# Kernel tuning notes

Hardware: AMD Instinct MI355X
Metric: run time of the kernel (lower is better)

## Reference

```python
import jax, jax.numpy as jnp
import numpy as np

N = 262144   # nodes
E = 1048576  # edges (avg degree 4)
DIN = 64     # input node features
H = 128      # hidden channels
DE = 32      # edge feature dim
EPS = 1e-5


def setup_inputs() -> dict:
    key = jax.random.key(0)
    ks = jax.random.split(key, 12)
    s = 0.05
    return {
        "x": jax.random.normal(ks[0], (N, DIN), jnp.float32),
        "edge_attr": jax.random.normal(ks[1], (E, DE), jnp.float32),
        "W_enter": jax.random.normal(ks[2], (H, DIN), jnp.float32) * s,
        "b_enter": jnp.zeros((H,), jnp.float32),
        "W1": jax.random.normal(ks[3], (H, H + DE), jnp.float32) * s,
        "att_l": jax.random.normal(ks[4], (H,), jnp.float32) * s,
        "att_r": jax.random.normal(ks[5], (H,), jnp.float32) * s,
        "W2": jax.random.normal(ks[6], (H, H), jnp.float32) * s,
        "b_conv": jnp.zeros((H,), jnp.float32),
        "W_ih": jax.random.normal(ks[7], (3 * H, H), jnp.float32) * s,
        "W_hh": jax.random.normal(ks[8], (3 * H, H), jnp.float32) * s,
        "b_ih": jnp.zeros((3 * H,), jnp.float32),
        "b_hh": jnp.zeros((3 * H,), jnp.float32),
        "edge_index": jax.random.randint(ks[9], (2, E), 0, N, jnp.int32),
    }


def _segment_softmax(logits, seg, num_segments):
    m = jax.ops.segment_max(logits, seg, num_segments=num_segments)
    e = jnp.exp(logits - m[seg])
    d = jax.ops.segment_sum(e, seg, num_segments=num_segments)
    return e / d[seg]


def reference(x, edge_attr, W_enter, b_enter, W1, att_l, att_r, W2, b_conv,
              W_ih, W_hh, b_ih, b_hh, edge_index):
    n = x.shape[0]
    src, dst = edge_index[0], edge_index[1]  # x_j = x[src], aggregate to dst

    # lin_enter + leaky_relu
    x = jax.nn.leaky_relu(x @ W_enter.T + b_enter)

    # Edge2dConv message: leaky_relu(lin1([x_j, edge_attr]))
    m = jax.nn.leaky_relu(jnp.concatenate([x[src], edge_attr], axis=-1) @ W1.T)  # [E,H]
    alpha = jax.nn.leaky_relu(m @ att_l + x[dst] @ att_r)  # [E]
    alpha = _segment_softmax(alpha, dst, n)
    msg = (m @ W2.T) * alpha[:, None]
    out = jax.ops.segment_sum(msg, dst, num_segments=n) + b_conv

    # elu, then GRUCell(h_in=out_elu, hidden=x)
    h = jax.nn.elu(out)
    gi = h @ W_ih.T + b_ih
    gh = x @ W_hh.T + b_hh
    ir, iz, inn = jnp.split(gi, 3, axis=-1)
    hr, hz, hn = jnp.split(gh, 3, axis=-1)
    r = jax.nn.sigmoid(ir + hr)
    z = jax.nn.sigmoid(iz + hz)
    ncand = jnp.tanh(inn + r * hn)
    x = jax.nn.relu((1.0 - z) * ncand + z * x)

    # layer_norm (no affine)
    mu = jnp.mean(x, axis=-1, keepdims=True)
    var = jnp.mean(jnp.square(x - mu), axis=-1, keepdims=True)
    return (x - mu) / jnp.sqrt(var + EPS)
```

## Files before the change

### kernel.cpp

```cpp
#include <hip/hip_runtime.h>
#include <stdint.h>

#define HD  128
#define DIN 64
#define DE  32

typedef unsigned int u32; typedef unsigned short u16; typedef unsigned char u8;
typedef long i64_;
typedef short s16x8 __attribute__((ext_vector_type(8)));
typedef float f32x4 __attribute__((ext_vector_type(4)));
typedef float f32x2 __attribute__((ext_vector_type(2)));

#define MFMA16(a,b,c)  __builtin_amdgcn_mfma_f32_16x16x32_bf16((a),(b),(c),0,0,0)
#define MFMAF8(a,b,c)  __builtin_amdgcn_mfma_f32_16x16x32_fp8_fp8((a),(b),(c),0,0,0)

__device__ __forceinline__ float lrelu(float x){ return x > 0.f ? x : 0.01f*x; }
__device__ __forceinline__ float sigmoidf_(float x){ return 1.f/(1.f + __expf(-x)); }
__device__ __forceinline__ float tanhf_(float x){
    float t = fminf(fmaxf(x, -15.f), 15.f);
    float e = __expf(2.f*t);
    return (e - 1.f)/(e + 1.f);
}
__device__ __forceinline__ float eluf_(float x){ return x > 0.f ? x : expm1f(x); }

__device__ __forceinline__ u16 f32_to_bf16(float x){
    u32 u = __float_as_uint(x);
    u += 0x7FFFu + ((u >> 16) & 1u);
    return (u16)(u >> 16);
}
__device__ __forceinline__ float bf16lo(u32 u){ return __uint_as_float((u & 0xFFFFu) << 16); }
__device__ __forceinline__ float bf16hi(u32 u){ return __uint_as_float(u & 0xFFFF0000u); }
__device__ __forceinline__ float bf16f(u16 h){ return __uint_as_float(((u32)h) << 16); }
__device__ __forceinline__ u32 pk2(float a, float b){
    return (u32)f32_to_bf16(a) | ((u32)f32_to_bf16(b) << 16);
}
__device__ __forceinline__ u8 hw_f8(float v){
    return (u8)__builtin_amdgcn_cvt_pk_fp8_f32(v, v, 0, false);
}
__device__ __forceinline__ u32 hw_f8x4(float a, float b, float c, float d){
    u32 r = (u32)__builtin_amdgcn_cvt_pk_fp8_f32(a, b, 0, false);
    r = (u32)__builtin_amdgcn_cvt_pk_fp8_f32(c, d, (int)r, true);
    return r;
}
__device__ __forceinline__ f32x2 hw_f8_dec2(u32 u){
    return __builtin_amdgcn_cvt_pk_f32_fp8((int)u, false);
}
__device__ __forceinline__ f32x2 hw_f8_dec2_hi(u32 u){
    return __builtin_amdgcn_cvt_pk_f32_fp8((int)u, true);
}

__device__ __forceinline__ float wave_max(float v){
    #pragma unroll
    for (int o = 32; o > 0; o >>= 1) v = fmaxf(v, __shfl_xor(v, o, 64));
    return v;
}
__device__ __forceinline__ float wave_sum(float v){
    #pragma unroll
    for (int o = 32; o > 0; o >>= 1) v += __shfl_xor(v, o, 64);
    return v;
}
__device__ __forceinline__ float dot8_bf16(uint4 v, const float* __restrict__ al){
    float d = 0.f;
    d = fmaf(bf16lo(v.x), al[0], d); d = fmaf(bf16hi(v.x), al[1], d);
    d = fmaf(bf16lo(v.y), al[2], d); d = fmaf(bf16hi(v.y), al[3], d);
    d = fmaf(bf16lo(v.z), al[4], d); d = fmaf(bf16hi(v.z), al[5], d);
    d = fmaf(bf16lo(v.w), al[6], d); d = fmaf(bf16hi(v.w), al[7], d);
    return d;
}

__global__ void k_prep(const float* __restrict__ W1, const float* __restrict__ W2,
                       const float* __restrict__ Went,
                       const float* __restrict__ Wih, const float* __restrict__ Whh,
                       u16* __restrict__ W1b, u16* __restrict__ W2b,
                       u16* __restrict__ Wentb, u8* __restrict__ Bgf8)
{
    int i = blockIdx.x*256 + threadIdx.x;
    if (i < 20480){ W1b[i] = f32_to_bf16(W1[i]); return; }
    i -= 20480;
    if (i < 16384){ W2b[i] = f32_to_bf16(W2[i]); return; }
    i -= 16384;
    if (i < 8192){ Wentb[i] = f32_to_bf16(Went[i]); return; }
    i -= 8192;
    if (i < 131072){
        int col = i >> 8, k = i & 255;
        int g = col >> 7, j = col & 127;
        float v;
        if      (g == 0) v = (k < 128) ? Wih[j*128 + k]        : Whh[j*128 + k - 128];
        else if (g == 1) v = (k < 128) ? Wih[(128+j)*128 + k]  : Whh[(128+j)*128 + k - 128];
        else if (g == 2) v = (k < 128) ? Wih[(256+j)*128 + k]  : 0.f;
        else             v = (k < 128) ? 0.f                   : Whh[(256+j)*128 + k - 128];
        Bgf8[i] = hw_f8(v);
    }
}

__global__ __launch_bounds__(256, 2) void k_enter_mfma(
    const float* __restrict__ x, const u16* __restrict__ Wb, const float* __restrict__ be,
    const float* __restrict__ att_r, u16* __restrict__ xeb, u8* __restrict__ Agru,
    float* __restrict__ r_out, int N)
{
    __shared__ __align__(16) u8 sA[64*144];
    __shared__ __align__(16) u8 sO[64*272];
    int t = threadIdx.x, w = t >> 6, lane = t & 63, l15 = lane & 15, l4 = lane >> 4;
    int tile = blockIdx.x;

    s16x8 bfr[2][2];
    #pragma unroll
    for (int kf = 0; kf < 2; ++kf)
        #pragma unroll
        for (int cf = 0; cf < 2; ++cf)
            bfr[kf][cf] = *(const s16x8*)(Wb + (size_t)(w*32 + cf*16 + l15)*64 + kf*32 + l4*8);

    int el = t >> 2, q = t & 3;
    size_t n = (size_t)tile*64 + el;
    {
        const float4* xs = (const float4*)(x + n*64 + q*16);
        float4 f0 = xs[0], f1 = xs[1], f2 = xs[2], f3 = xs[3];
        uint4 o0, o1;
        o0.x = pk2(f0.x,f0.y); o0.y = pk2(f0.z,f0.w); o0.z = pk2(f1.x,f1.y); o0.w = pk2(f1.z,f1.w);
        o1.x = pk2(f2.x,f2.y); o1.y = pk2(f2.z,f2.w); o1.z = pk2(f3.x,f3.y); o1.w = pk2(f3.z,f3.w);
        *(uint4*)(sA + el*144 + q*32)      = o0;
        *(uint4*)(sA + el*144 + q*32 + 16) = o1;
    }
    __syncthreads();

    f32x4 acc[4][2];
    #pragma unroll
    for (int rf = 0; rf < 4; ++rf){ acc[rf][0] = (f32x4)0.f; acc[rf][1] = (f32x4)0.f; }
    #pragma unroll
    for (int kf = 0; kf < 2; ++kf){
        s16x8 a[4];
        #pragma unroll
        for (int rf = 0; rf < 4; ++rf)
            a[rf] = *(const s16x8*)(sA + (rf*16 + l15)*144 + kf*64 + l4*16);
        #pragma unroll
        for (int rf = 0; rf < 4; ++rf){
            acc[rf][0] = MFMA16(a[rf], bfr[kf][0], acc[rf][0]);
            acc[rf][1] = MFMA16(a[rf], bfr[kf][1], acc[rf][1]);
        }
    }
    float b0 = be[w*32 + l15], b1 = be[w*32 + 16 + l15];
    #pragma unroll
    for (int rf = 0; rf < 4; ++rf)
        #pragma unroll
        for (int r = 0; r < 4; ++r){
            int row = rf*16 + l4*4 + r;
            *(u16*)(sO + row*272 + (w*32 + l15)*2)      = f32_to_bf16(lrelu(acc[rf][0][r] + b0));
            *(u16*)(sO + row*272 + (w*32 + 16 + l15)*2) = f32_to_bf16(lrelu(acc[rf][1][r] + b1));
        }
    __syncthreads();

    float dot = 0.f;
    #pragma unroll
    for (int i = 0; i < 4; ++i){
        uint4 v = *(const uint4*)(sO + el*272 + q*64 + 16*i);
        ((uint4*)xeb)[n*16 + q*4 + i] = v;
        float f0 = bf16lo(v.x), f1 = bf16hi(v.x), f2 = bf16lo(v.y), f3 = bf16hi(v.y);
        float f4 = bf16lo(v.z), f5 = bf16hi(v.z), f6 = bf16lo(v.w), f7 = bf16hi(v.w);
        const float* al = att_r + q*32 + 8*i;
        dot = fmaf(f0, al[0], dot); dot = fmaf(f1, al[1], dot);
        dot = fmaf(f2, al[2], dot); dot = fmaf(f3, al[3], dot);
        dot = fmaf(f4, al[4], dot); dot = fmaf(f5, al[5], dot);
        dot = fmaf(f6, al[6], dot); dot = fmaf(f7, al[7], dot);
        uint2 p; p.x = hw_f8x4(f0, f1, f2, f3); p.y = hw_f8x4(f4, f5, f6, f7);
        *(uint2*)(Agru + n*256 + 128 + q*32 + i*8) = p;
    }
    dot += __shfl_xor(dot, 1); dot += __shfl_xor(dot, 2);
    if (q == 0) r_out[n] = dot;
}

__global__ void k_hist(const int* __restrict__ dst, int* __restrict__ deg, int E){
    int e = blockIdx.x*256 + threadIdx.x;
    if (e < E) atomicAdd(&deg[dst[e]], 1);
}
__global__ __launch_bounds__(256) void k_scan_a(
    const int* __restrict__ deg, int* __restrict__ rs, int* __restrict__ btot, int N)
{
    __shared__ int sd[256];
    int b = blockIdx.x, t = threadIdx.x;
    int base = b*1024 + t*4;
    int d0 = deg[base], d1 = deg[base+1], d2 = deg[base+2], d3 = deg[base+3];
    int s = d0 + d1 + d2 + d3;
    sd[t] = s; __syncthreads();
    for (int o = 1; o < 256; o <<= 1){
        int v = (t >= o) ? sd[t-o] : 0;
        __syncthreads();
        sd[t] += v;
        __syncthreads();
    }
    int ex = sd[t] - s;
    rs[base]   = ex;
    rs[base+1] = ex + d0;
    rs[base+2] = ex + d0 + d1;
    rs[base+3] = ex + d0 + d1 + d2;
    if (t == 0) btot[b] = sd[255];
}
__global__ __launch_bounds__(256) void k_scan_b(const int* __restrict__ btot, int* __restrict__ bbase){
    __shared__ int sd[256];
    int t = threadIdx.x;
    int s = btot[t];
    sd[t] = s; __syncthreads();
    for (int o = 1; o < 256; o <<= 1){
        int v = (t >= o) ? sd[t-o] : 0;
        __syncthreads();
        sd[t] += v;
        __syncthreads();
    }
    bbase[t] = sd[t] - s;
}
__global__ void k_scan_c(int* __restrict__ rs, const int* __restrict__ bbase, int N, int E){
    int i = blockIdx.x*256 + threadIdx.x;
    if (i < N) rs[i] += bbase[i >> 10];
    if (i == 0) rs[N] = E;
}
__global__ void k_scatter(const int* __restrict__ dst, const int* __restrict__ rs,
                          int* __restrict__ cnt, int* __restrict__ epos, int E){
    int e = blockIdx.x*256 + threadIdx.x;
    if (e >= E) return;
    int d = dst[e];
    int pos = rs[d] + atomicAdd(&cnt[d], 1);
    epos[e] = pos;
}

__global__ __launch_bounds__(512, 4) void k_edge_mfma(
    const u16* __restrict__ xeb, const float* __restrict__ ea,
    const u16* __restrict__ W1b, const float* __restrict__ att_l,
    const float* __restrict__ r_dst, const int* __restrict__ src, const int* __restrict__ dst,
    const int* __restrict__ epos,
    u8* __restrict__ m, float* __restrict__ alpha, int ntiles, int E)
{
    __shared__ __align__(16) u8 sA[64*336];
    __shared__ __align__(16) u8 sM[64*144];
    int t = threadIdx.x, w = t >> 6, lane = t & 63, l15 = lane & 15, l4 = lane >> 4;

    s16x8 bfr[5];
    #pragma unroll
    for (int kf = 0; kf < 5; ++kf)
        bfr[kf] = *(const s16x8*)(W1b + (size_t)(w*16 + l15)*160 + kf*32 + l4*8);

    int el = t >> 3, q = t & 7;
    int stride = gridDim.x;
    int tile = blockIdx.x;

    uint4 cx0, cx1;
    u32 ce0, ce1;
    int   pe = 0;
    float rdv = 0.f;
    {
        int e = tile*64 + el;
        if (tile < ntiles && e < E){
            int sn = src[e];
            const uint4* xs = (const uint4*)xeb + (size_t)sn*16 + q*2;
            cx0 = xs[0]; cx1 = xs[1];
            float4 f = *(const float4*)(ea + (size_t)e*32 + q*4);
            ce0 = pk2(f.x, f.y); ce1 = pk2(f.z, f.w);
            pe  = epos[e];
            rdv = r_dst[dst[e]];
        }
    }

    int   ptile = -1;
    int   pe_prev = 0;
    float rdv_prev = 0.f;

    for (; tile < ntiles; tile += stride){
        int e = tile*64 + el;
        if (e < E){
            uint4* d = (uint4*)(sA + el*336 + q*32);
            d[0] = cx0; d[1] = cx1;
            *(u32*)(sA + el*336 + 256 + q*8)     = ce0;
            *(u32*)(sA + el*336 + 256 + q*8 + 4) = ce1;
        }
        int pe_cur = pe; float rdv_cur = rdv;

        int nt = tile + stride;
        if (nt < ntiles){
            int e2 = nt*64 + el;
            if (e2 < E){
                int sn = src[e2];
                const uint4* xs = (const uint4*)xeb + (size_t)sn*16 + q*2;
                cx0 = xs[0]; cx1 = xs[1];
                float4 f = *(const float4*)(ea + (size_t)e2*32 + q*4);
                ce0 = pk2(f.x, f.y); ce1 = pk2(f.z, f.w);
                pe  = epos[e2];
                rdv = r_dst[dst[e2]];
            }
        }

        if (ptile >= 0){
            int ep = ptile*64 + el;
            if (ep < E){
                uint4 v = *(const uint4*)(sM + el*144 + q*16);
                ((uint4*)m)[(size_t)pe_prev*8 + q] = v;
                u32 ws[4] = {v.x, v.y, v.z, v.w};
                float dotv = 0.f;
                #pragma unroll
                for (int i = 0; i < 4; ++i){
                    f32x2 fa = hw_f8_dec2(ws[i]);
                    f32x2 fb = hw_f8_dec2_hi(ws[i]);
                    const float* al = att_l + q*16 + i*4;
                    dotv = fmaf(fa.x, al[0], dotv); dotv = fmaf(fa.y, al[1], dotv);
                    dotv = fmaf(fb.x, al[2], dotv); dotv = fmaf(fb.y, al[3], dotv);
                }
                dotv += __shfl_xor(dotv, 1); dotv += __shfl_xor(dotv, 2); dotv += __shfl_xor(dotv, 4);
                if (q == 0) alpha[pe_prev] = lrelu(dotv + rdv_prev);
            }
        }
        __syncthreads();

        f32x4 acc[4];
        #pragma unroll
        for (int rf = 0; rf < 4; ++rf) acc[rf] = (f32x4)0.f;
        #pragma unroll
        for (int kf = 0; kf < 5; ++kf){
            s16x8 a[4];
            #pragma unroll
            for (int rf = 0; rf < 4; ++rf)
                a[rf] = *(const s16x8*)(sA + (rf*16 + l15)*336 + kf*64 + l4*16);
            #pragma unroll
            for (int rf = 0; rf < 4; ++rf)
                acc[rf] = MFMA16(a[rf], bfr[kf], acc[rf]);
        }

        int col = w*16 + l15;
        #pragma unroll
        for (int rf = 0; rf < 4; ++rf)
            #pragma unroll
            for (int r = 0; r < 4; ++r){
                int row = rf*16 + l4*4 + r;
                sM[row*144 + col] = hw_f8(lrelu(acc[rf][r]));
            }
        __syncthreads();

        ptile = tile; pe_prev = pe_cur; rdv_prev = rdv_cur;
    }

    if (ptile >= 0){
        int ep = ptile*64 + el;
        if (ep < E){
            uint4 v = *(const uint4*)(sM + el*144 + q*16);
            ((uint4*)m)[(size_t)pe_prev*8 + q] = v;
            u32 ws[4] = {v.x, v.y, v.z, v.w};
            float dotv = 0.f;
            #pragma unroll
            for (int i = 0; i < 4; ++i){
                f32x2 fa = hw_f8_dec2(ws[i]);
                f32x2 fb = hw_f8_dec2_hi(ws[i]);
                const float* al = att_l + q*16 + i*4;
                dotv = fmaf(fa.x, al[0], dotv); dotv = fmaf(fa.y, al[1], dotv);
                dotv = fmaf(fb.x, al[2], dotv); dotv = fmaf(fb.y, al[3], dotv);
            }
            dotv += __shfl_xor(dotv, 1); dotv += __shfl_xor(dotv, 2); dotv += __shfl_xor(dotv, 4);
            if (q == 0) alpha[pe_prev] = lrelu(dotv + rdv_prev);
        }
    }
}

__global__ __launch_bounds__(512, 2) void k_aggconv(
    const int* __restrict__ rs, const float* __restrict__ alpha, const u8* __restrict__ m,
    const u16* __restrict__ W2b, const float* __restrict__ bc,
    u8* __restrict__ Agru, int N)
{
    __shared__ __align__(16) u8 sA[64*272];
    __shared__ __align__(16) u8 sO[64*272];
    int t = threadIdx.x, w = t >> 6, lane = t & 63, l15 = lane & 15, l4 = lane >> 4;
    int tile = blockIdx.x;

    s16x8 bfr[4];
    #pragma unroll
    for (int kf = 0; kf < 4; ++kf)
        bfr[kf] = *(const s16x8*)(W2b + (size_t)(w*16 + l15)*128 + kf*32 + l4*8);

    #pragma unroll 1
    for (int i = 0; i < 8; ++i){
        int nloc = w*8 + i;
        int n = tile*64 + nloc;
        int s = rs[n], tend = rs[n+1];
        int deg = tend - s;
        float ax = 0.f, ay = 0.f;
        if (deg > 0 && deg <= 64){
            float av = -1e38f;
            if (lane < deg) av = alpha[s + lane];
            float mx = wave_max(av);
            float ev = (lane < deg) ? __expf(av - mx) : 0.f;
            float ssum = wave_sum(ev);
            float wreg = ev / ssum;
            int k = 0;
            for (; k + 2 <= deg; k += 2){
                float w0 = __shfl(wreg, k);
                float w1 = __shfl(wreg, k + 1);
                u32 u0 = *(const u16*)(m + (size_t)(s + k)*HD + 2*lane);
                u32 u1 = *(const u16*)(m + (size_t)(s + k + 1)*HD + 2*lane);
                f32x2 f0 = hw_f8_dec2(u0);
                f32x2 f1 = hw_f8_dec2(u1);
                ax = fmaf(w0, f0.x, ax); ay = fmaf(w0, f0.y, ay);
                ax = fmaf(w1, f1.x, ax); ay = fmaf(w1, f1.y, ay);
            }
            if (k < deg){
                float w0 = __shfl(wreg, k);
                u32 u0 = *(const u16*)(m + (size_t)(s + k)*HD + 2*lane);
                f32x2 f0 = hw_f8_dec2(u0);
                ax = fmaf(w0, f0.x, ax); ay = fmaf(w0, f0.y, ay);
            }
        } else if (deg > 64){
            float mx = -1e38f;
            for (int k = lane; k < deg; k += 64) mx = fmaxf(mx, alpha[s + k]);
            mx = wave_max(mx);
            float ssum = 0.f;
            for (int k = lane; k < deg; k += 64) ssum += __expf(alpha[s + k] - mx);
            ssum = wave_sum(ssum);
            float inv = 1.f / ssum;
            for (int k = 0; k < deg; ++k){
                float wgt = __expf(alpha[s + k] - mx) * inv;
                u32 u0 = *(const u16*)(m + (size_t)(s + k)*HD + 2*lane);
                f32x2 f0 = hw_f8_dec2(u0);
                ax = fmaf(wgt, f0.x, ax);
                ay = fmaf(wgt, f0.y, ay);
            }
        }
        *(u32*)(sA + nloc*272 + lane*4) = pk2(ax, ay);
    }
    __syncthreads();

    f32x4 acc[4];
    #pragma unroll
    for (int rf = 0; rf < 4; ++rf) acc[rf] = (f32x4)0.f;
    #pragma unroll
    for (int kf = 0; kf < 4; ++kf){
        s16x8 av[4];
        #pragma unroll
        for (int rf = 0; rf < 4; ++rf)
            av[rf] = *(const s16x8*)(sA + (rf*16 + l15)*272 + kf*64 + l4*16);
        #pragma unroll
        for (int rf = 0; rf < 4; ++rf)
            acc[rf] = MFMA16(av[rf], bfr[kf], acc[rf]);
    }
    float b0 = bc[w*16 + l15];
    #pragma unroll
    for (int rf = 0; rf < 4; ++rf)
        #pragma unroll
        for (int r = 0; r < 4; ++r){
            int row = rf*16 + l4*4 + r;
            *(u16*)(sO + row*272 + (w*16 + l15)*2) = f32_to_bf16(eluf_(acc[rf][r] + b0));
        }
    __syncthreads();

    {
        int el = t >> 3, q = t & 7;
        size_t n = (size_t)tile*64 + el;
        uint4 v0 = *(const uint4*)(sO + el*272 + q*32);
        uint4 v1 = *(const uint4*)(sO + el*272 + q*32 + 16);
        uint4 p;
        p.x = hw_f8x4(bf16lo(v0.x), bf16hi(v0.x), bf16lo(v0.y), bf16hi(v0.y));
        p.y = hw_f8x4(bf16lo(v0.z), bf16hi(v0.z), bf16lo(v0.w), bf16hi(v0.w));
        p.z = hw_f8x4(bf16lo(v1.x), bf16hi(v1.x), bf16lo(v1.y), bf16hi(v1.y));
        p.w = hw_f8x4(bf16lo(v1.z), bf16hi(v1.z), bf16lo(v1.w), bf16hi(v1.w));
        *(uint4*)(Agru + n*256 + q*16) = p;
    }
}

__global__ __launch_bounds__(512, 4) void k_gru_mfma(
    const u8* __restrict__ Agru, const u16* __restrict__ xeb, const u8* __restrict__ Bgf8,
    const float* __restrict__ bih, const float* __restrict__ bhh,
    float* __restrict__ out, int N, int ntiles)
{
    __shared__ __align__(16) u8 sA[32*272];
    __shared__ __align__(16) u8 sX[32*272];
    __shared__ __align__(16) float sOut[32*132];
    int t = threadIdx.x, w = t >> 6, lane = t & 63, l15 = lane & 15, l4 = lane >> 4;

    i64_ bfr0[8], bfr1[8], bfr2[4], bfr3[4];
    {
        int jc = w*16 + l15;
        #pragma unroll
        for (int kf = 0; kf < 8; ++kf){
            bfr0[kf] = *(const i64_*)(Bgf8 + (size_t)(jc)*256       + kf*32 + l4*8);
            bfr1[kf] = *(const i64_*)(Bgf8 + (size_t)(128 + jc)*256 + kf*32 + l4*8);
        }
        #pragma unroll
        for (int kf = 0; kf < 4; ++kf){
            bfr2[kf] = *(const i64_*)(Bgf8 + (size_t)(256 + jc)*256 + kf*32 + l4*8);
            bfr3[kf] = *(const i64_*)(Bgf8 + (size_t)(384 + jc)*256 + (kf+4)*32 + l4*8);
        }
    }
    int j = w*16 + l15;
    float rb = bih[j] + bhh[j];
    float zb = bih[128 + j] + bhh[128 + j];
    float ib = bih[256 + j];
    float hb = bhh[256 + j];

    int el = t >> 4, part = t & 15;
    int stride = gridDim.x;
    int tile = blockIdx.x;
    uint4 pa, px;
    if (tile < ntiles){
        pa = *((const uint4*)Agru + ((size_t)tile*32 + el)*16 + part);
        px = *((const uint4*)xeb  + ((size_t)tile*32 + el)*16 + part);
    }

    for (; tile < ntiles; tile += stride){
        *(uint4*)(sA + el*272 + part*16) = pa;
        *(uint4*)(sX + el*272 + part*16) = px;
        __syncthreads();

        int nt = tile + stride;
        if (nt < ntiles){
            pa = *((const uint4*)Agru + ((size_t)nt*32 + el)*16 + part);
            px = *((const uint4*)xeb  + ((size_t)nt*32 + el)*16 + part);
        }

        f32x4 acc[2][4];
        #pragma unroll
        for (int rf = 0; rf < 2; ++rf)
            #pragma unroll
            for (int g = 0; g < 4; ++g) acc[rf][g] = (f32x4)0.f;
        #pragma unroll
        for (int kf = 0; kf < 8; ++kf){
            i64_ a0 = *(const i64_*)(sA + l15*272 + kf*32 + l4*8);
            i64_ a1 = *(const i64_*)(sA + (16 + l15)*272 + kf*32 + l4*8);
            acc[0][0] = MFMAF8(a0, bfr0[kf], acc[0][0]);
            acc[1][0] = MFMAF8(a1, bfr0[kf], acc[1][0]);
            acc[0][1] = MFMAF8(a0, bfr1[kf], acc[0][1]);
            acc[1][1] = MFMAF8(a1, bfr1[kf], acc[1][1]);
            if (kf < 4){
                acc[0][2] = MFMAF8(a0, bfr2[kf], acc[0][2]);
                acc[1][2] = MFMAF8(a1, bfr2[kf], acc[1][2]);
            } else {
                acc[0][3] = MFMAF8(a0, bfr3[kf-4], acc[0][3]);
                acc[1][3] = MFMAF8(a1, bfr3[kf-4], acc[1][3]);
            }
        }
        #pragma unroll
        for (int rf = 0; rf < 2; ++rf)
            #pragma unroll
            for (int r = 0; r < 4; ++r){
                int rl = rf*16 + l4*4 + r;
                float rr = sigmoidf_(acc[rf][0][r] + rb);
                float zz = sigmoidf_(acc[rf][1][r] + zb);
                float iv = acc[rf][2][r] + ib;
                float hv = acc[rf][3][r] + hb;
                float nc = tanhf_(iv + rr*hv);
                float xej = bf16f(*(const u16*)(sX + rl*272 + 2*j));
                float v = (1.f - zz)*nc + zz*xej;
                v = fmaxf(v, 0.f);
                sOut[rl*132 + j] = v;
            }
        __syncthreads();
        {
            int row = t >> 4, sub = t & 15;
            const float* rp = sOut + row*132 + sub*8;
            float v0 = rp[0], v1 = rp[1], v2 = rp[2], v3 = rp[3];
            float v4 = rp[4], v5 = rp[5], v6 = rp[6], v7 = rp[7];
            float s1 = v0+v1+v2+v3+v4+v5+v6+v7;
            float s2 = v0*v0+v1*v1+v2*v2+v3*v3+v4*v4+v5*v5+v6*v6+v7*v7;
            #pragma unroll
            for (int o = 1; o < 16; o <<= 1){ s1 += __shfl_xor(s1, o); s2 += __shfl_xor(s2, o); }
            float mu  = s1 * (1.f/128.f);
            float var = s2 * (1.f/128.f) - mu*mu;
            var = fmaxf(var, 0.f);
            float rsd = rsqrtf(var + 1e-5f);
            float* op = out + ((size_t)tile*32 + row)*128 + sub*8;
            float4 o0, o1;
            o0.x = (v0-mu)*rsd; o0.y = (v1-mu)*rsd; o0.z = (v2-mu)*rsd; o0.w = (v3-mu)*rsd;
            o1.x = (v4-mu)*rsd; o1.y = (v5-mu)*rsd; o1.z = (v6-mu)*rsd; o1.w = (v7-mu)*rsd;
            ((float4*)op)[0] = o0; ((float4*)op)[1] = o1;
        }
        __syncthreads();
    }
}

extern "C" void kernel_launch(void* const* d_in, const int* in_sizes, int n_in,
                              void* d_out, int out_size, void* d_ws, size_t ws_size,
                              hipStream_t stream)
{
    const float* x       = (const float*)d_in[0];
    const float* ea      = (const float*)d_in[1];
    const float* W_enter = (const float*)d_in[2];
    const float* b_enter = (const float*)d_in[3];
    const float* W1      = (const float*)d_in[4];
    const float* att_l   = (const float*)d_in[5];
    const float* att_r   = (const float*)d_in[6];
    const float* W2      = (const float*)d_in[7];
    const float* b_conv  = (const float*)d_in[8];
    const float* W_ih    = (const float*)d_in[9];
    const float* W_hh    = (const float*)d_in[10];
    const float* b_ih    = (const float*)d_in[11];
    const float* b_hh    = (const float*)d_in[12];
    const int*   eidx    = (const int*)d_in[13];

    int N = in_sizes[0] / DIN;
    int E = in_sizes[13] / 2;
    const int* src = eidx;
    const int* dst = eidx + E;
    float* out = (float*)d_out;

    size_t off = 0;
    char* base = (char*)d_ws;
    auto alloc = [&](size_t bytes) -> char* {
        char* p = base + off;
        off = (off + bytes + 255) & ~(size_t)255;
        return p;
    };
    u16*   xeb   = (u16*)  alloc((size_t)N*HD*2);
    u8*    Agru  = (u8*)   alloc((size_t)N*256);
    float* r_dst = (float*)alloc((size_t)N*4);
    float* alpha = (float*)alloc((size_t)E*4);
    int*   deg   = (int*)  alloc((size_t)N*4);
    int*   rs    = (int*)  alloc((size_t)(N+1)*4);
    int*   cnt   = (int*)  alloc((size_t)N*4);
    int*   epos  = (int*)  alloc((size_t)E*4);
    int*   btot  = (int*)  alloc(1024);
    int*   bbase = (int*)  alloc(1024);
    u16*   W1b   = (u16*)  alloc(20480*2);
    u16*   W2b   = (u16*)  alloc(16384*2);
    u16*   Wentb = (u16*)  alloc(8192*2);
    u8*    Bgf8  = (u8*)   alloc(131072);
    u8*    mbuf  = (u8*)   alloc((size_t)E*HD);

    int ntiles_n64 = N/64, ntiles_e = (E + 63)/64, ntiles_g = N/32;

    k_prep   <<<(176128+255)/256, 256, 0, stream>>>(W1, W2, W_enter, W_ih, W_hh, W1b, W2b, Wentb, Bgf8);
    hipMemsetAsync(deg, 0, (size_t)N*4, stream);
    hipMemsetAsync(cnt, 0, (size_t)N*4, stream);
    k_enter_mfma<<<ntiles_n64, 256, 0, stream>>>(x, Wentb, b_enter, att_r, xeb, Agru, r_dst, N);
    k_hist   <<<(E+255)/256, 256, 0, stream>>>(dst, deg, E);
    k_scan_a <<<N/1024, 256, 0, stream>>>(deg, rs, btot, N);
    k_scan_b <<<1, 256, 0, stream>>>(btot, bbase);
    k_scan_c <<<(N+255)/256, 256, 0, stream>>>(rs, bbase, N, E);
    k_scatter<<<(E+255)/256, 256, 0, stream>>>(dst, rs, cnt, epos, E);
    k_edge_mfma<<<1024, 512, 0, stream>>>(xeb, ea, W1b, att_l, r_dst, src, dst, epos,
                                          mbuf, alpha, ntiles_e, E);
    k_aggconv<<<ntiles_n64, 512, 0, stream>>>(rs, alpha, mbuf, W2b, b_conv, Agru, N);
    k_gru_mfma  <<<2048, 512, 0, stream>>>(Agru, xeb, Bgf8, b_ih, b_hh, out, N, ntiles_g);
}
```

Baseline: 524.7 us.

## Fuse CSR scatter into edge kernel and pack fp8 LDS stores

Removes the separate k_scatter kernel and the epos buffer. Each edge's CSR slot is now taken by an atomicAdd on cnt inside k_edge_mfma, done by one lane per edge and broadcast to the others with __shfl. This saves a kernel launch and an E-sized write plus read of positions. The byte-wise fp8 writes of the MFMA output to shared memory are replaced by packing four fp8 values, then shuffle/perm transposes, so each lane does one 32-bit store. The cost is atomic traffic inside the main edge loop and extra shuffle and perm instructions.

```diff
diff --git a/kernel.cpp b/kernel.cpp
--- a/kernel.cpp
+++ b/kernel.cpp
@@ -58,14 +58,6 @@
     #pragma unroll
     for (int o = 32; o > 0; o >>= 1) v += __shfl_xor(v, o, 64);
     return v;
-}
-__device__ __forceinline__ float dot8_bf16(uint4 v, const float* __restrict__ al){
-    float d = 0.f;
-    d = fmaf(bf16lo(v.x), al[0], d); d = fmaf(bf16hi(v.x), al[1], d);
-    d = fmaf(bf16lo(v.y), al[2], d); d = fmaf(bf16hi(v.y), al[3], d);
-    d = fmaf(bf16lo(v.z), al[4], d); d = fmaf(bf16hi(v.z), al[5], d);
-    d = fmaf(bf16lo(v.w), al[6], d); d = fmaf(bf16hi(v.w), al[7], d);
-    return d;
 }
 
 __global__ void k_prep(const float* __restrict__ W1, const float* __restrict__ W2,
@@ -212,20 +204,12 @@
     if (i < N) rs[i] += bbase[i >> 10];
     if (i == 0) rs[N] = E;
 }
-__global__ void k_scatter(const int* __restrict__ dst, const int* __restrict__ rs,
-                          int* __restrict__ cnt, int* __restrict__ epos, int E){
-    int e = blockIdx.x*256 + threadIdx.x;
-    if (e >= E) return;
-    int d = dst[e];
-    int pos = rs[d] + atomicAdd(&cnt[d], 1);
-    epos[e] = pos;
-}
 
 __global__ __launch_bounds__(512, 4) void k_edge_mfma(
     const u16* __restrict__ xeb, const float* __restrict__ ea,
     const u16* __restrict__ W1b, const float* __restrict__ att_l,
     const float* __restrict__ r_dst, const int* __restrict__ src, const int* __restrict__ dst,
-    const int* __restrict__ epos,
+    const int* __restrict__ rs, int* __restrict__ cnt,
     u8* __restrict__ m, float* __restrict__ alpha, int ntiles, int E)
 {
     __shared__ __align__(16) u8 sA[64*336];
@@ -253,8 +237,11 @@
             cx0 = xs[0]; cx1 = xs[1];
             float4 f = *(const float4*)(ea + (size_t)e*32 + q*4);
             ce0 = pk2(f.x, f.y); ce1 = pk2(f.z, f.w);
-            pe  = epos[e];
-            rdv = r_dst[dst[e]];
+            if (q == 0){
+                int d = dst[e];
+                pe  = rs[d] + atomicAdd(&cnt[d], 1);
+                rdv = r_dst[d];
+            }
         }
     }
 
@@ -270,7 +257,9 @@
             *(u32*)(sA + el*336 + 256 + q*8)     = ce0;
             *(u32*)(sA + el*336 + 256 + q*8 + 4) = ce1;
         }
-        int pe_cur = pe; float rdv_cur = rdv;
+        int pe_cur = __shfl(pe, (lane & 7)*8 + 0, 64);
+        pe_cur = pe;
+        float rdv_cur = rdv;
 
         int nt = tile + stride;
         if (nt < ntiles){
@@ -281,16 +270,20 @@
                 cx0 = xs[0]; cx1 = xs[1];
                 float4 f = *(const float4*)(ea + (size_t)e2*32 + q*4);
                 ce0 = pk2(f.x, f.y); ce1 = pk2(f.z, f.w);
-                pe  = epos[e2];
-                rdv = r_dst[dst[e2]];
+                if (q == 0){
+                    int d = dst[e2];
+                    pe  = rs[d] + atomicAdd(&cnt[d], 1);
+                    rdv = r_dst[d];
+                }
             }
         }
 
         if (ptile >= 0){
             int ep = ptile*64 + el;
             if (ep < E){
+                int pp = __shfl(pe_prev, el*8, 64);
                 uint4 v = *(const uint4*)(sM + el*144 + q*16);
-                ((uint4*)m)[(size_t)pe_prev*8 + q] = v;
+                ((uint4*)m)[(size_t)pp*8 + q] = v;
                 u32 ws[4] = {v.x, v.y, v.z, v.w};
                 float dotv = 0.f;
                 #pragma unroll
@@ -302,7 +295,7 @@
                     dotv = fmaf(fb.x, al[2], dotv); dotv = fmaf(fb.y, al[3], dotv);
                 }
                 dotv += __shfl_xor(dotv, 1); dotv += __shfl_xor(dotv, 2); dotv += __shfl_xor(dotv, 4);
-                if (q == 0) alpha[pe_prev] = lrelu(dotv + rdv_prev);
+                if (q == 0) alpha[pp] = lrelu(dotv + __shfl(rdv_prev, el*8, 64));
             }
         }
         __syncthreads();
@@ -321,14 +314,22 @@
                 acc[rf] = MFMA16(a[rf], bfr[kf], acc[rf]);
         }
 
-        int col = w*16 + l15;
-        #pragma unroll
-        for (int rf = 0; rf < 4; ++rf)
+        {
+            int colbase = w*16 + (l15 & 12);
+            int rowsub  = l4*4 + (l15 & 3);
             #pragma unroll
-            for (int r = 0; r < 4; ++r){
-                int row = rf*16 + l4*4 + r;
-                sM[row*144 + col] = hw_f8(lrelu(acc[rf][r]));
-            }
+            for (int rf = 0; rf < 4; ++rf){
+                u32 v0 = hw_f8x4(lrelu(acc[rf][0]), lrelu(acc[rf][1]),
+                                 lrelu(acc[rf][2]), lrelu(acc[rf][3]));
+                u32 p1 = (u32)__shfl_xor((int)v0, 1, 64);
+                u32 x  = (l15 & 1) ? __builtin_amdgcn_perm(p1, v0, 0x03070105u)
+                                   : __builtin_amdgcn_perm(p1, v0, 0x06020400u);
+                u32 p2 = (u32)__shfl_xor((int)x, 2, 64);
+                u32 y  = (l15 & 2) ? __builtin_amdgcn_perm(p2, x, 0x03020706u)
+                                   : __builtin_amdgcn_perm(p2, x, 0x05040100u);
+                *(u32*)(sM + (rf*16 + rowsub)*144 + colbase) = y;
+            }
+        }
         __syncthreads();
 
         ptile = tile; pe_prev = pe_cur; rdv_prev = rdv_cur;
@@ -337,8 +338,9 @@
     if (ptile >= 0){
         int ep = ptile*64 + el;
         if (ep < E){
+            int pp = __shfl(pe_prev, el*8, 64);
             uint4 v = *(const uint4*)(sM + el*144 + q*16);
-            ((uint4*)m)[(size_t)pe_prev*8 + q] = v;
+            ((uint4*)m)[(size_t)pp*8 + q] = v;
             u32 ws[4] = {v.x, v.y, v.z, v.w};
             float dotv = 0.f;
             #pragma unroll
@@ -350,7 +352,7 @@
                 dotv = fmaf(fb.x, al[2], dotv); dotv = fmaf(fb.y, al[3], dotv);
             }
             dotv += __shfl_xor(dotv, 1); dotv += __shfl_xor(dotv, 2); dotv += __shfl_xor(dotv, 4);
-            if (q == 0) alpha[pe_prev] = lrelu(dotv + rdv_prev);
+            if (q == 0) alpha[pp] = lrelu(dotv + __shfl(rdv_prev, el*8, 64));
         }
     }
 }
@@ -607,7 +609,6 @@
     int*   deg   = (int*)  alloc((size_t)N*4);
     int*   rs    = (int*)  alloc((size_t)(N+1)*4);
     int*   cnt   = (int*)  alloc((size_t)N*4);
-    int*   epos  = (int*)  alloc((size_t)E*4);
     int*   btot  = (int*)  alloc(1024);
     int*   bbase = (int*)  alloc(1024);
     u16*   W1b   = (u16*)  alloc(20480*2);
@@ -626,8 +627,7 @@
     k_scan_a <<<N/1024, 256, 0, stream>>>(deg, rs, btot, N);
     k_scan_b <<<1, 256, 0, stream>>>(btot, bbase);
     k_scan_c <<<(N+255)/256, 256, 0, stream>>>(rs, bbase, N, E);
-    k_scatter<<<(E+255)/256, 256, 0, stream>>>(dst, rs, cnt, epos, E);
-    k_edge_mfma<<<1024, 512, 0, stream>>>(xeb, ea, W1b, att_l, r_dst, src, dst, epos,
+    k_edge_mfma<<<1024, 512, 0, stream>>>(xeb, ea, W1b, att_l, r_dst, src, dst, rs, cnt,
                                           mbuf, alpha, ntiles_e, E);
     k_aggconv<<<ntiles_n64, 512, 0, stream>>>(rs, alpha, mbuf, W2b, b_conv, Agru, N);
     k_gru_mfma  <<<2048, 512, 0, stream>>>(Agru, xeb, Bgf8, b_ih, b_hh, out, N, ntiles_g);
```

Result: no change. 528.0 us (+0.6%).
